# Performance work log

Hardware: AMD Instinct MI355X
Metric: run time of the kernel (lower is better)

The kernel has to match this reference:

```python
import jax, jax.numpy as jnp
import numpy as np

B, T, Z, AE, H, M, A = 32, 512, 128, 16, 1024, 5, 18
OUT = Z * 3 * M + 1  # 1921
K = M * Z  # per-component split size for logmix/mu/logstd


def setup_inputs() -> dict:
    key = jax.random.key(0)
    ks = jax.random.split(key, 9)
    s = 0.02
    return {
        "z": jax.random.normal(ks[0], (B, T, Z), jnp.float32),
        "actions": jax.random.randint(ks[1], (B, T), 0, A, jnp.int32),
        "dones": jax.random.randint(ks[2], (B, T), 0, 2, jnp.int32),
        "embed": jax.random.normal(ks[3], (A, AE), jnp.float32) * s,
        "W_ih": jax.random.normal(ks[4], (4 * H, Z + AE), jnp.float32) * s,
        "W_hh": jax.random.normal(ks[5], (4 * H, H), jnp.float32) * s,
        "b_ih": jnp.zeros((4 * H,), jnp.float32),
        "b_hh": jnp.zeros((4 * H,), jnp.float32),
        "W_out": jax.random.normal(ks[6], (OUT, H), jnp.float32) * s,
        "b_out": jnp.zeros((OUT,), jnp.float32),
    }


def reference(z, actions, dones, embed, W_ih, W_hh, b_ih, b_hh, W_out, b_out):
    a_emb = embed[actions]                              # [B,T,AE]
    inp = jnp.concatenate([z, a_emb], axis=2)           # [B,T,Z+AE]
    d = dones.astype(inp.dtype)                         # [B,T]
    # precompute input contribution to gates for all timesteps (one big GEMM)
    x_pre = jnp.einsum('btf,gf->btg', inp, W_ih) + b_ih + b_hh  # [B,T,4H]

    def cell(carry, xt):
        h, c = carry
        xg, dt = xt                                     # xg: [B,4H], dt: [B]
        gates = xg + h @ W_hh.T
        i, f, g, o = jnp.split(gates, 4, axis=1)        # torch LSTMCell order i,f,g,o
        c_new = jax.nn.sigmoid(f) * c + jax.nn.sigmoid(i) * jnp.tanh(g)
        h_new = jax.nn.sigmoid(o) * jnp.tanh(c_new)
        mask = (1.0 - dt)[:, None]                      # done-masking AFTER output
        return (h_new * mask, c_new * mask), h_new

    h0 = jnp.zeros((B, H), inp.dtype)
    _, hs = jax.lax.scan(cell, (h0, h0), (x_pre.transpose(1, 0, 2), d.T))
    hs = hs.transpose(1, 0, 2)[:, :-1]                  # [B,T-1,H]
    out = hs @ W_out.T + b_out                          # [B,T-1,OUT]

    logmix = out[..., :K].reshape(-1, M)
    mu = out[..., K:2 * K].reshape(-1, M)
    logstd = out[..., 2 * K:3 * K].reshape(-1, M)
    done_p = out[..., 3 * K:].squeeze(-1)               # [B,T-1]
    logmix = logmix - jax.scipy.special.logsumexp(logmix, axis=1, keepdims=True)
    return logmix, mu, logstd, done_p
```

## Files before the change

kernel.cpp:

```cpp
#include <hip/hip_runtime.h>
#include <hip/hip_bf16.h>


typedef float f4 __attribute__((ext_vector_type(4)));
typedef short s8 __attribute__((ext_vector_type(8)));
typedef unsigned short us8v __attribute__((ext_vector_type(8)));
typedef unsigned short us4v __attribute__((ext_vector_type(4)));
typedef unsigned long long u64;
typedef unsigned u32;

#define DEV __device__ __forceinline__

DEV unsigned short f2b(float f) {
  unsigned u = __float_as_uint(f);
  return (unsigned short)((u + 0x7FFFu + ((u >> 16) & 1u)) >> 16);
}
DEV float b2f(unsigned short s) { return __uint_as_float(((unsigned)s) << 16); }

DEV f4 MFMA(s8 a, s8 b, f4 c) {
  return __builtin_amdgcn_mfma_f32_16x16x32_bf16(a, b, c, 0, 0, 0);
}
DEV s8 LD8(const unsigned short* p) { return *reinterpret_cast<const s8*>(p); }

DEV u32 AL32(const u32* p) {
  return __hip_atomic_load(p, __ATOMIC_RELAXED, __HIP_MEMORY_SCOPE_AGENT);
}
DEV void AS(u64* p, u64 v) {
  __hip_atomic_store(p, v, __ATOMIC_RELAXED, __HIP_MEMORY_SCOPE_AGENT);
}

DEV float sigf(float x) {
  float e = __builtin_amdgcn_exp2f(x * -1.44269504f);
  return __builtin_amdgcn_rcpf(1.f + e);
}
DEV float tanhf_fast(float x) {
  float e = __builtin_amdgcn_exp2f(x * 2.88539008f);
  return 1.f - 2.f * __builtin_amdgcn_rcpf(e + 1.f);
}

static constexpr size_t WS_GCNT = 0;
static constexpr size_t WS_NACT = 2048;
static constexpr size_t WS_HDR  = 4096;
static constexpr size_t WS_META = 4352;
static constexpr size_t WS_LOFF = 69888;
static constexpr size_t WS_TMP  = 131072;
static constexpr size_t WS_ZT   = 131072;
static constexpr size_t WS_WOUT = 4325376;
static constexpr size_t WS_HS2  = 8261632;
static constexpr size_t WS_END  = 41816064;
static constexpr size_t DO_CALL = 35651584;

__global__ void cvt_wout_k(const float* __restrict__ W, unsigned short* __restrict__ o) {
  int i = blockIdx.x * 256 + threadIdx.x;
  if (i < 491776) {
    const float4 v = reinterpret_cast<const float4*>(W)[i];
    us4v u; u[0] = f2b(v.x); u[1] = f2b(v.y); u[2] = f2b(v.z); u[3] = f2b(v.w);
    reinterpret_cast<us4v*>(o)[i] = u;
  }
}

__global__ void cvt_z_k(const float* __restrict__ z, unsigned short* __restrict__ zt) {
  int i = blockIdx.x * 256 + threadIdx.x;
  if (i < 524288) {
    const float4 v = reinterpret_cast<const float4*>(z)[i];
    us4v u; u[0] = f2b(v.x); u[1] = f2b(v.y); u[2] = f2b(v.z); u[3] = f2b(v.w);
    reinterpret_cast<us4v*>(zt)[i] = u;
  }
}

__global__ void zero_hs_tail_k(u64* __restrict__ hs2) {
  int i = blockIdx.x * 256 + threadIdx.x;
  if (i < 8192) {
    int region = i >> 6, rr = (i & 63) >> 1, hf = i & 1;
    hs2[((size_t)region * 16384 + 16352 + rr) * 2 + hf] = 0ull;
  }
}

__global__ __launch_bounds__(256) void seg_build_k(
    const int* __restrict__ dones, u32* __restrict__ tmp,
    u32* __restrict__ meta, u32* __restrict__ nact, u32* __restrict__ hdr,
    u32* __restrict__ loff) {
  __shared__ u32 hist[512];
  __shared__ u32 cur[512];
  __shared__ u32 scnt[32];
  const int tid = threadIdx.x;
  for (int i = tid; i < 512; i += 256) hist[i] = 0;
  __syncthreads();
  if (tid < 32) {
    int b = tid, cnt = 0, t0 = 0;
    for (int t = 1; t <= 511; ++t) {
      bool brk = (t == 511) || (dones[b * 512 + t - 1] != 0);
      if (brk) {
        int len = t - t0;
        tmp[b * 511 + cnt] = ((u32)t0 << 16) | (u32)len;
        atomicAdd(&hist[len], 1u);
        ++cnt; t0 = t;
      }
    }
    scnt[b] = (u32)cnt;
  }
  __syncthreads();
  if (tid == 0) {
    u32 acc = 0; int ml = 0;
    for (int L = 511; L >= 0; --L) {
      cur[L] = acc; nact[L] = acc;
      if (hist[L] && !ml) ml = L;
      acc += hist[L];
    }
    hdr[0] = acc; hdr[1] = (u32)ml;
    u32 off = 0; loff[0] = 0;
    for (int s2 = 1; s2 <= ml; ++s2) { loff[s2] = off; off += nact[s2]; }
  }
  __syncthreads();
  if (tid < 32) {
    int b = tid; u32 c = scnt[b];
    for (u32 i = 0; i < c; ++i) {
      u32 e = tmp[b * 511 + i];
      u32 len = e & 0xFFFFu, t0 = e >> 16;
      u32 slot = atomicAdd(&cur[len], 1u);
      meta[slot] = ((u32)b << 20) | (t0 << 10) | len;
    }
  }
}

__global__ __launch_bounds__(512, 1) void lstm_seg_k(
    const float* __restrict__ Whh, const float* __restrict__ Wih,
    const float* __restrict__ embed, const float* __restrict__ bih,
    const float* __restrict__ bhh, const int* __restrict__ actions,
    const unsigned short* __restrict__ zt, const u32* __restrict__ meta,
    const u32* __restrict__ nact, const u32* __restrict__ hdr,
    const u32* __restrict__ loff, u64* __restrict__ hsl,
    u64* __restrict__ c_all, u64* __restrict__ hs2,
    u32* __restrict__ gcnt) {
  const int blk = blockIdx.x;
  const int g = blk >> 1;
  const int half = blk & 1;
  const int tid = threadIdx.x;
  const int lane = tid & 63;
  const int w = tid >> 6;
  const int ln = lane & 15, lk = lane >> 4;

  __shared__ alignas(16) unsigned short whh_sw[32 * 2 * 64 * 8];
  __shared__ alignas(16) unsigned short wz_sw[4 * 2 * 64 * 8];
  __shared__ float abias[18][32];
  __shared__ float red[8][64][33];

  for (int i = tid; i < 32768; i += 512) {
    int j = i & 7, L = (i >> 3) & 63, nt = (i >> 9) & 1, kt = i >> 10;
    int n = nt * 16 + (L & 15);
    int grow = (n >> 3) * 1024 + g * 8 + (n & 7);
    int k = kt * 32 + ((L >> 4) << 3) + j;
    whh_sw[i] = f2b(Whh[grow * 1024 + k]);
  }
  for (int i = tid; i < 4096; i += 512) {
    int j = i & 7, L = (i >> 3) & 63, nt = (i >> 9) & 1, kz = i >> 10;
    int n = nt * 16 + (L & 15);
    int grow = (n >> 3) * 1024 + g * 8 + (n & 7);
    int k = kz * 32 + ((L >> 4) << 3) + j;
    wz_sw[i] = f2b(Wih[grow * 144 + k]);
  }
  for (int i = tid; i < 18 * 32; i += 512) {
    int a = i >> 5, n = i & 31;
    int grow = (n >> 3) * 1024 + g * 8 + (n & 7);
    float s = bih[grow] + bhh[grow];
    for (int j = 0; j < 16; ++j) s += embed[a * 16 + j] * Wih[grow * 144 + 128 + j];
    abias[a][n] = s;
  }
  __syncthreads();

  const int maxlen = (int)hdr[1];

  for (int s = 0; s < maxlen; ++s) {
    const u32 N = nact[s];
    const int ntiles = (int)((N + 63) >> 6);
    const u64* hread = hsl + (size_t)loff[s] * 256;
    u64* hwrite = hsl + (size_t)loff[s + 1] * 256;

    for (int tile = half + 2 * w; tile < ntiles; tile += 16) {
      const u32 sb = (u32)tile << 6;
      const u32 slot = sb + (u32)lane;
      const bool valid = slot < N;
      const u32 m = valid ? meta[slot] : 0u;
      const u32 b = m >> 20, t0 = (m >> 10) & 1023u, L = m & 1023u;
      const int zrow = (int)(b * 512u + t0 + (u32)s);
      const int orow = (int)(b * 511u + t0 + (u32)s);
      const u32 act = valid ? (u32)actions[zrow] : 0u;
      u64 cq[4] = {0, 0, 0, 0};
      if (s && valid) {
        const u64* cp = c_all + ((size_t)blk << 15) + ((size_t)slot << 2);
        cq[0] = cp[0]; cq[1] = cp[1]; cq[2] = cp[2]; cq[3] = cp[3];
      }
      int zr[4];
#pragma unroll
      for (int q = 0; q < 4; ++q) zr[q] = __shfl(zrow, ln + 16 * q, 64);

      f4 a00 = {0,0,0,0}, a01 = {0,0,0,0}, a10 = {0,0,0,0}, a11 = {0,0,0,0};
      f4 a20 = {0,0,0,0}, a21 = {0,0,0,0}, a30 = {0,0,0,0}, a31 = {0,0,0,0};
#pragma unroll
      for (int kz = 0; kz < 4; ++kz) {
        s8 b0 = LD8(wz_sw + (((kz * 2 + 0) * 64 + lane) << 3));
        s8 b1 = LD8(wz_sw + (((kz * 2 + 1) * 64 + lane) << 3));
        s8 f0 = LD8(zt + (size_t)zr[0] * 128 + kz * 32 + (lk << 3));
        s8 f1 = LD8(zt + (size_t)zr[1] * 128 + kz * 32 + (lk << 3));
        s8 f2 = LD8(zt + (size_t)zr[2] * 128 + kz * 32 + (lk << 3));
        s8 f3 = LD8(zt + (size_t)zr[3] * 128 + kz * 32 + (lk << 3));
        a00 = MFMA(f0, b0, a00);  a01 = MFMA(f0, b1, a01);
        a10 = MFMA(f1, b0, a10);  a11 = MFMA(f1, b1, a11);
        a20 = MFMA(f2, b0, a20);  a21 = MFMA(f2, b1, a21);
        a30 = MFMA(f3, b0, a30);  a31 = MFMA(f3, b1, a31);
      }
      if (s) {
        const u32 r0c = (sb + (u32)ln      < N) ? sb + (u32)ln      : N - 1u;
        const u32 r1c = (sb + (u32)ln + 16 < N) ? sb + (u32)ln + 16 : N - 1u;
        const u32 r2c = (sb + (u32)ln + 32 < N) ? sb + (u32)ln + 32 : N - 1u;
        const u32 r3c = (sb + (u32)ln + 48 < N) ? sb + (u32)ln + 48 : N - 1u;
        const unsigned short* h0 =
            (const unsigned short*)(hread + (size_t)r0c * 256) + (lk << 3);
        const unsigned short* h1 =
            (const unsigned short*)(hread + (size_t)r1c * 256) + (lk << 3);
        const unsigned short* h2 =
            (const unsigned short*)(hread + (size_t)r2c * 256) + (lk << 3);
        const unsigned short* h3 =
            (const unsigned short*)(hread + (size_t)r3c * 256) + (lk << 3);
#pragma unroll 8
        for (int kt = 0; kt < 32; ++kt) {
          s8 b0 = LD8(whh_sw + (((kt * 2 + 0) * 64 + lane) << 3));
          s8 b1 = LD8(whh_sw + (((kt * 2 + 1) * 64 + lane) << 3));
          s8 f0 = LD8(h0 + (kt << 5));
          s8 f1 = LD8(h1 + (kt << 5));
          s8 f2 = LD8(h2 + (kt << 5));
          s8 f3 = LD8(h3 + (kt << 5));
          a00 = MFMA(f0, b0, a00);  a01 = MFMA(f0, b1, a01);
          a10 = MFMA(f1, b0, a10);  a11 = MFMA(f1, b1, a11);
          a20 = MFMA(f2, b0, a20);  a21 = MFMA(f2, b1, a21);
          a30 = MFMA(f3, b0, a30);  a31 = MFMA(f3, b1, a31);
        }
      }

#pragma unroll
      for (int j = 0; j < 4; ++j) {
        red[w][(lk << 2) + j][ln]           = a00[j];
        red[w][(lk << 2) + j][16 + ln]      = a01[j];
        red[w][16 + (lk << 2) + j][ln]      = a10[j];
        red[w][16 + (lk << 2) + j][16 + ln] = a11[j];
        red[w][32 + (lk << 2) + j][ln]      = a20[j];
        red[w][32 + (lk << 2) + j][16 + ln] = a21[j];
        red[w][48 + (lk << 2) + j][ln]      = a30[j];
        red[w][48 + (lk << 2) + j][16 + ln] = a31[j];
      }
      const bool carry = valid && (L > (u32)(s + 1));
      u32 cb[8]; unsigned short hb[8];
#pragma unroll
      for (int e = 0; e < 8; ++e) {
        float gi = red[w][lane][e]      + abias[act][e];
        float gf = red[w][lane][8 + e]  + abias[act][8 + e];
        float gg = red[w][lane][16 + e] + abias[act][16 + e];
        float go = red[w][lane][24 + e] + abias[act][24 + e];
        const u32 cpb = (e & 1) ? (u32)(cq[e >> 1] >> 32) : (u32)cq[e >> 1];
        const float cprev = __uint_as_float(cpb);
        const float si = sigf(gi), sf = sigf(gf), so = sigf(go);
        const float cn = sf * cprev + si * tanhf_fast(gg);
        const float hn = so * tanhf_fast(cn);
        cb[e] = __float_as_uint(cn);
        hb[e] = f2b(hn);
      }
      if (carry) {
        u64* cp = c_all + ((size_t)blk << 15) + ((size_t)slot << 2);
        cp[0] = ((u64)cb[1] << 32) | (u64)cb[0];
        cp[1] = ((u64)cb[3] << 32) | (u64)cb[2];
        cp[2] = ((u64)cb[5] << 32) | (u64)cb[4];
        cp[3] = ((u64)cb[7] << 32) | (u64)cb[6];
      }
      const u64 hu0 = (u64)hb[0] | ((u64)hb[1] << 16) |
                      ((u64)hb[2] << 32) | ((u64)hb[3] << 48);
      const u64 hu1 = (u64)hb[4] | ((u64)hb[5] << 16) |
                      ((u64)hb[6] << 32) | ((u64)hb[7] << 48);
      if (valid) {
        u64* hp = hs2 + ((size_t)g * 16384 + orow) * 2;
        hp[0] = hu0; hp[1] = hu1;
        if (carry) {
          AS(hwrite + (size_t)slot * 256 + 2 * g, hu0);
          AS(hwrite + (size_t)slot * 256 + 2 * g + 1, hu1);
        }
      }
    }

    asm volatile("s_waitcnt vmcnt(0)" ::: "memory");
    __syncthreads();
    if (s + 1 < maxlen) {
      if (tid == 0) {
        __hip_atomic_fetch_add(gcnt + (blk >> 4) * 32, 1u,
                               __ATOMIC_RELAXED, __HIP_MEMORY_SCOPE_AGENT);
        const u32 tgt = (u32)(s + 1) * 16u;
        for (u32 spin = 0; spin < (1u << 20); ++spin) {
          u32 mn = 0xFFFFFFFFu;
#pragma unroll
          for (int gg2 = 0; gg2 < 16; ++gg2) {
            u32 v = AL32(gcnt + gg2 * 32);
            mn = (v < mn) ? v : mn;
          }
          if (mn >= tgt) break;
          __builtin_amdgcn_s_sleep(1);
        }
      }
      __syncthreads();
    }
  }
}

__global__ __launch_bounds__(256, 2) void out_gemm_k(
    const u64* __restrict__ hs2, const unsigned short* __restrict__ wout,
    const float* __restrict__ b_out, float* __restrict__ out) {
  const int mblk = blockIdx.x, nblk = blockIdx.y;
  const int tid = threadIdx.x, lane = tid & 63, w = tid >> 6;
  const int ln = lane & 15, lk = lane >> 4;
  __shared__ alignas(16) unsigned char smraw[26112];
  unsigned short* bsm = (unsigned short*)smraw;
  float* ep = (float*)smraw;
  const bool last = (nblk == 23);

  if (last) {
    for (int i = tid; i < 15 * 136; i += 256) bsm[81 * 136 + i] = 0;
  }
  __syncthreads();

  const int r0 = mblk * 64 + w * 16;
  f4 acc[5];
#pragma unroll
  for (int s = 0; s < 5; ++s) acc[s] = (f4){0.f, 0.f, 0.f, 0.f};
  f4 acc5 = {0.f, 0.f, 0.f, 0.f};

  for (int kc = 0; kc < 8; ++kc) {
#pragma unroll
    for (int ii = 0; ii < 5; ++ii) {
      int i = tid + ii * 256;
      int n = i >> 4, k16 = i & 15;
      us8v v = *reinterpret_cast<const us8v*>(
          wout + (size_t)(nblk * 80 + n) * 1024 + kc * 128 + (k16 << 3));
      *reinterpret_cast<us8v*>(bsm + n * 136 + (k16 << 3)) = v;
    }
    if (last && tid < 16) {
      us8v v = *reinterpret_cast<const us8v*>(
          wout + (size_t)1920 * 1024 + kc * 128 + (tid << 3));
      *reinterpret_cast<us8v*>(bsm + 80 * 136 + (tid << 3)) = v;
    }
    __syncthreads();
#pragma unroll
    for (int ks = 0; ks < 4; ++ks) {
      const int k0 = kc * 128 + ks * 32 + (lk << 3);
      s8 a = *reinterpret_cast<const s8*>(
          hs2 + ((size_t)(k0 >> 3) * 16384 + r0 + ln) * 2);
#pragma unroll
      for (int s = 0; s < 5; ++s) {
        s8 b = LD8(bsm + (s * 16 + ln) * 136 + ks * 32 + (lk << 3));
        acc[s] = MFMA(a, b, acc[s]);
      }
      if (last) {
        s8 b6 = LD8(bsm + ((80 + ln) * 136) + ks * 32 + (lk << 3));
        acc5 = MFMA(a, b6, acc5);
      }
    }
    __syncthreads();
  }

  const int T = nblk >> 3;
  if (T) {
    float* base = out + (size_t)10465280 * T;
    const int lc0 = (nblk - (T << 3)) * 80;
#pragma unroll
    for (int s = 0; s < 5; ++s) {
      const int lc = lc0 + s * 16 + ln;
      const float bias = b_out[T * 640 + lc];
#pragma unroll
      for (int j = 0; j < 4; ++j) {
        const int row = r0 + (lk << 2) + j;
        if (row < 16352) base[(size_t)row * 640 + lc] = acc[s][j] + bias;
      }
    }
    if (last && ln == 0) {
      const float bias = b_out[1920];
#pragma unroll
      for (int j = 0; j < 4; ++j) {
        const int row = r0 + (lk << 2) + j;
        if (row < 16352) out[31395840 + row] = acc5[j] + bias;
      }
    }
  } else {
#pragma unroll
    for (int s = 0; s < 5; ++s) {
      const float bias = b_out[nblk * 80 + s * 16 + ln];
#pragma unroll
      for (int j = 0; j < 4; ++j)
        ep[(w * 16 + (lk << 2) + j) * 84 + s * 16 + ln] = acc[s][j] + bias;
    }
    __syncthreads();
    for (int task = tid; task < 1024; task += 256) {
      const int rr = task >> 4, grp = task & 15;
      const int row = mblk * 64 + rr;
      const float* e = ep + rr * 84 + grp * 5;
      float v0 = e[0], v1 = e[1], v2 = e[2], v3 = e[3], v4 = e[4];
      float mx = fmaxf(fmaxf(fmaxf(v0, v1), fmaxf(v2, v3)), v4);
      float ssum = expf(v0 - mx) + expf(v1 - mx) + expf(v2 - mx) +
                   expf(v3 - mx) + expf(v4 - mx);
      float lse = mx + logf(ssum);
      if (row < 16352) {
        float* o = out + (size_t)row * 640 + nblk * 80 + grp * 5;
        o[0] = v0 - lse; o[1] = v1 - lse; o[2] = v2 - lse;
        o[3] = v3 - lse; o[4] = v4 - lse;
      }
    }
  }
}

extern "C" void kernel_launch(void* const* d_in, const int* in_sizes, int n_in,
                              void* d_out, int out_size, void* d_ws, size_t ws_size,
                              hipStream_t stream) {
  const float* z       = (const float*)d_in[0];
  const int*   actions = (const int*)d_in[1];
  const int*   dones   = (const int*)d_in[2];
  const float* embed   = (const float*)d_in[3];
  const float* Wih     = (const float*)d_in[4];
  const float* Whh     = (const float*)d_in[5];
  const float* bih     = (const float*)d_in[6];
  const float* bhh     = (const float*)d_in[7];
  const float* Wout    = (const float*)d_in[8];
  const float* bout    = (const float*)d_in[9];
  float* out = (float*)d_out;

  if (ws_size < WS_END) return;

  char* ws = (char*)d_ws;
  u32* gcnt              = (u32*)(ws + WS_GCNT);
  u32* nact              = (u32*)(ws + WS_NACT);
  u32* hdr               = (u32*)(ws + WS_HDR);
  u32* metaA             = (u32*)(ws + WS_META);
  u32* loff              = (u32*)(ws + WS_LOFF);
  u32* tmp               = (u32*)(ws + WS_TMP);
  unsigned short* zt     = (unsigned short*)(ws + WS_ZT);
  unsigned short* wout16 = (unsigned short*)(ws + WS_WOUT);
  u64* hs2               = (u64*)(ws + WS_HS2);
  u64* hsl   = (u64*)d_out;
  u64* call  = (u64*)((char*)d_out + DO_CALL);

  hipMemsetAsync(d_ws, 0, 2048, stream);

  seg_build_k<<<1, 256, 0, stream>>>(dones, tmp, metaA, nact, hdr, loff);
  cvt_z_k<<<2048, 256, 0, stream>>>(z, zt);
  zero_hs_tail_k<<<32, 256, 0, stream>>>(hs2);
  lstm_seg_k<<<256, 512, 0, stream>>>(Whh, Wih, embed, bih, bhh, actions,
                                      zt, metaA, nact, hdr, loff, hsl, call,
                                      hs2, gcnt);
  cvt_wout_k<<<1921, 256, 0, stream>>>(Wout, wout16);
  out_gemm_k<<<dim3(256, 24), 256, 0, stream>>>(hs2, wout16, bout, out);
}
```

Baseline: 863.6 us.

## Double LSTM block to 1024 threads with phased per-quarter LDS gate reduction

The recurrent LSTM kernel now runs 16 waves per block instead of 8, and each block walks tiles with a stride of 32. To fit the extra waves in LDS, the per-wave scratch buffer shrinks from 64x33 to 16x33 floats. The reduction is split into four phases, and in each phase only the 16 lanes owning that row group compute the gate nonlinearities. This trades 4x-serialized gate math inside each wave for twice as many concurrent tiles per CU, aiming to hide latency in the per-step recurrent loop.

```diff
diff --git a/kernel.cpp b/kernel.cpp
--- a/kernel.cpp
+++ b/kernel.cpp
@@ -123,7 +123,7 @@
   }
 }
 
-__global__ __launch_bounds__(512, 1) void lstm_seg_k(
+__global__ __launch_bounds__(1024, 1) void lstm_seg_k(
     const float* __restrict__ Whh, const float* __restrict__ Wih,
     const float* __restrict__ embed, const float* __restrict__ bih,
     const float* __restrict__ bhh, const int* __restrict__ actions,
@@ -139,27 +139,28 @@
   const int lane = tid & 63;
   const int w = tid >> 6;
   const int ln = lane & 15, lk = lane >> 4;
+  const int lq = lane >> 4, lr = lane & 15;
 
   __shared__ alignas(16) unsigned short whh_sw[32 * 2 * 64 * 8];
   __shared__ alignas(16) unsigned short wz_sw[4 * 2 * 64 * 8];
   __shared__ float abias[18][32];
-  __shared__ float red[8][64][33];
-
-  for (int i = tid; i < 32768; i += 512) {
+  __shared__ float red16[16][16][33];
+
+  for (int i = tid; i < 32768; i += 1024) {
     int j = i & 7, L = (i >> 3) & 63, nt = (i >> 9) & 1, kt = i >> 10;
     int n = nt * 16 + (L & 15);
     int grow = (n >> 3) * 1024 + g * 8 + (n & 7);
     int k = kt * 32 + ((L >> 4) << 3) + j;
     whh_sw[i] = f2b(Whh[grow * 1024 + k]);
   }
-  for (int i = tid; i < 4096; i += 512) {
+  for (int i = tid; i < 4096; i += 1024) {
     int j = i & 7, L = (i >> 3) & 63, nt = (i >> 9) & 1, kz = i >> 10;
     int n = nt * 16 + (L & 15);
     int grow = (n >> 3) * 1024 + g * 8 + (n & 7);
     int k = kz * 32 + ((L >> 4) << 3) + j;
     wz_sw[i] = f2b(Wih[grow * 144 + k]);
   }
-  for (int i = tid; i < 18 * 32; i += 512) {
+  for (int i = tid; i < 18 * 32; i += 1024) {
     int a = i >> 5, n = i & 31;
     int grow = (n >> 3) * 1024 + g * 8 + (n & 7);
     float s = bih[grow] + bhh[grow];
@@ -176,7 +177,7 @@
     const u64* hread = hsl + (size_t)loff[s] * 256;
     u64* hwrite = hsl + (size_t)loff[s + 1] * 256;
 
-    for (int tile = half + 2 * w; tile < ntiles; tile += 16) {
+    for (int tile = half + 2 * w; tile < ntiles; tile += 32) {
       const u32 sb = (u32)tile << 6;
       const u32 slot = sb + (u32)lane;
       const bool valid = slot < N;
@@ -237,33 +238,37 @@
         }
       }
 
-#pragma unroll
-      for (int j = 0; j < 4; ++j) {
-        red[w][(lk << 2) + j][ln]           = a00[j];
-        red[w][(lk << 2) + j][16 + ln]      = a01[j];
-        red[w][16 + (lk << 2) + j][ln]      = a10[j];
-        red[w][16 + (lk << 2) + j][16 + ln] = a11[j];
-        red[w][32 + (lk << 2) + j][ln]      = a20[j];
-        red[w][32 + (lk << 2) + j][16 + ln] = a21[j];
-        red[w][48 + (lk << 2) + j][ln]      = a30[j];
-        red[w][48 + (lk << 2) + j][16 + ln] = a31[j];
-      }
       const bool carry = valid && (L > (u32)(s + 1));
       u32 cb[8]; unsigned short hb[8];
-#pragma unroll
-      for (int e = 0; e < 8; ++e) {
-        float gi = red[w][lane][e]      + abias[act][e];
-        float gf = red[w][lane][8 + e]  + abias[act][8 + e];
-        float gg = red[w][lane][16 + e] + abias[act][16 + e];
-        float go = red[w][lane][24 + e] + abias[act][24 + e];
-        const u32 cpb = (e & 1) ? (u32)(cq[e >> 1] >> 32) : (u32)cq[e >> 1];
-        const float cprev = __uint_as_float(cpb);
-        const float si = sigf(gi), sf = sigf(gf), so = sigf(go);
-        const float cn = sf * cprev + si * tanhf_fast(gg);
-        const float hn = so * tanhf_fast(cn);
-        cb[e] = __float_as_uint(cn);
-        hb[e] = f2b(hn);
-      }
+#define PHASE(Q, A0, A1)                                                    \
+      {                                                                     \
+        _Pragma("unroll") for (int j = 0; j < 4; ++j) {                     \
+          red16[w][(lk << 2) + j][ln]      = A0[j];                         \
+          red16[w][(lk << 2) + j][16 + ln] = A1[j];                         \
+        }                                                                   \
+        if (lq == Q) {                                                      \
+          _Pragma("unroll") for (int e = 0; e < 8; ++e) {                   \
+            float gi = red16[w][lr][e]      + abias[act][e];                \
+            float gf = red16[w][lr][8 + e]  + abias[act][8 + e];            \
+            float gg = red16[w][lr][16 + e] + abias[act][16 + e];           \
+            float go = red16[w][lr][24 + e] + abias[act][24 + e];           \
+            const u32 cpb = (e & 1) ? (u32)(cq[e >> 1] >> 32)               \
+                                    : (u32)cq[e >> 1];                      \
+            const float cprev = __uint_as_float(cpb);                       \
+            const float si = sigf(gi), sf = sigf(gf), so = sigf(go);        \
+            const float cn = sf * cprev + si * tanhf_fast(gg);              \
+            const float hn = so * tanhf_fast(cn);                           \
+            cb[e] = __float_as_uint(cn);                                    \
+            hb[e] = f2b(hn);                                                \
+          }                                                                 \
+        }                                                                   \
+      }
+      PHASE(0, a00, a01)
+      PHASE(1, a10, a11)
+      PHASE(2, a20, a21)
+      PHASE(3, a30, a31)
+#undef PHASE
+
       if (carry) {
         u64* cp = c_all + ((size_t)blk << 15) + ((size_t)slot << 2);
         cp[0] = ((u64)cb[1] << 32) | (u64)cb[0];
@@ -447,9 +452,9 @@
   seg_build_k<<<1, 256, 0, stream>>>(dones, tmp, metaA, nact, hdr, loff);
   cvt_z_k<<<2048, 256, 0, stream>>>(z, zt);
   zero_hs_tail_k<<<32, 256, 0, stream>>>(hs2);
-  lstm_seg_k<<<256, 512, 0, stream>>>(Whh, Wih, embed, bih, bhh, actions,
-                                      zt, metaA, nact, hdr, loff, hsl, call,
-                                      hs2, gcnt);
+  lstm_seg_k<<<256, 1024, 0, stream>>>(Whh, Wih, embed, bih, bhh, actions,
+                                       zt, metaA, nact, hdr, loff, hsl, call,
+                                       hs2, gcnt);
   cvt_wout_k<<<1921, 256, 0, stream>>>(Wout, wout16);
   out_gemm_k<<<dim3(256, 24), 256, 0, stream>>>(hs2, wout16, bout, out);
 }
```

Result: slower. 954.4 us (+10.5%).
